# Kernel tuning notes

Hardware: AMD Instinct MI355X
Metric: run time of the kernel (lower is better)

The kernel has to match this reference:

```python
import jax, jax.numpy as jnp
import numpy as np

NUM_HEADS = 16
ROPE_BASE = 10000.0


def _rope_interleaved(x, cos, sin):
    # x: (B, S, H, hd); cos/sin: (1, S, 1, hd//2)
    x1 = x[..., ::2]
    x2 = x[..., 1::2]
    r1 = x1 * cos - x2 * sin
    r2 = x1 * sin + x2 * cos
    return jnp.stack([r1, r2], axis=-1).reshape(x.shape)


def _rope_tables(seq_len, head_dim, dtype):
    dim = head_dim // 2
    freqs = jnp.exp(-jnp.arange(0, dim, dtype=dtype) * jnp.log(jnp.asarray(ROPE_BASE, dtype)) / dim)
    pos = jnp.arange(seq_len, dtype=dtype)
    angles = pos[:, None] * freqs[None, :]  # (S, hd//2)
    return jnp.cos(angles)[None, :, None, :], jnp.sin(angles)[None, :, None, :]


def setup_inputs() -> dict:
    key = jax.random.key(0)
    ks = jax.random.split(key, 9)
    B, S, D = 2, 2048, 2048
    sc = 1.0 / np.sqrt(D)
    return {
        "x": jax.random.normal(ks[0], (B, S, D), jnp.float32),
        "wq": jax.random.normal(ks[1], (D, D), jnp.float32) * sc,
        "bq": jax.random.normal(ks[2], (D,), jnp.float32) * 0.01,
        "wk": jax.random.normal(ks[3], (D, D), jnp.float32) * sc,
        "bk": jax.random.normal(ks[4], (D,), jnp.float32) * 0.01,
        "wv": jax.random.normal(ks[5], (D, D), jnp.float32) * sc,
        "bv": jax.random.normal(ks[6], (D,), jnp.float32) * 0.01,
        "wo": jax.random.normal(ks[7], (D, D), jnp.float32) * sc,
        "bo": jax.random.normal(ks[8], (D,), jnp.float32) * 0.01,
    }


def reference(x, wq, bq, wk, bk, wv, bv, wo, bo):
    B, S, D = x.shape
    H = NUM_HEADS
    hd = D // H
    # QKV projections (eqx.nn.Linear: y = W @ x + b, weight (out, in))
    q = (x @ wq.T + bq).reshape(B, S, H, hd)
    k = (x @ wk.T + bk).reshape(B, S, H, hd)
    v = (x @ wv.T + bv).reshape(B, S, H, hd)
    # RoPE (interleaved / GPT-NeoX style)
    cos, sin = _rope_tables(S, hd, x.dtype)
    q = _rope_interleaved(q, cos, sin)
    k = _rope_interleaved(k, cos, sin)
    # Causal scaled dot-product attention
    scale = 1.0 / np.sqrt(hd)
    scores = jnp.einsum("bqhd,bkhd->bhqk", q, k) * scale
    causal = jnp.tril(jnp.ones((S, S), dtype=bool))
    scores = jnp.where(causal[None, None, :, :], scores, jnp.finfo(scores.dtype).min)
    attn = jax.nn.softmax(scores, axis=-1)
    out = jnp.einsum("bhqk,bkhd->bqhd", attn, v).reshape(B, S, D)
    return out @ wo.T + bo
```

## Files before the change

### kernel.cpp

```cpp
#include <hip/hip_runtime.h>

typedef unsigned short u16;
typedef short bf16x8 __attribute__((ext_vector_type(8)));
typedef float f32x4 __attribute__((ext_vector_type(4)));

#define B_ 2
#define S_ 2048
#define D_ 2048
#define HD_ 128
#define GW 512
#define KB 64
#define VST 72
#define PST 72

__device__ __forceinline__ float bf2f(u16 h) {
  unsigned u = ((unsigned)h) << 16;
  return __builtin_bit_cast(float, u);
}
__device__ __forceinline__ u16 f2bf(float f) {
  unsigned u = __builtin_bit_cast(unsigned, f);
  u += 0x7FFF + ((u >> 16) & 1);
  return (u16)(u >> 16);
}
__device__ __forceinline__ bf16x8 cvt8(const float* p) {
  float4 a = *(const float4*)p;
  float4 b = *(const float4*)(p + 4);
  bf16x8 r;
  r[0] = (short)f2bf(a.x); r[1] = (short)f2bf(a.y);
  r[2] = (short)f2bf(a.z); r[3] = (short)f2bf(a.w);
  r[4] = (short)f2bf(b.x); r[5] = (short)f2bf(b.y);
  r[6] = (short)f2bf(b.z); r[7] = (short)f2bf(b.w);
  return r;
}

__device__ __forceinline__ void gload16(const void* g, void* lds) {
  __builtin_amdgcn_global_load_lds(
      (const __attribute__((address_space(1))) unsigned*)g,
      (__attribute__((address_space(3))) unsigned*)lds, 16, 0, 0);
}

__device__ __forceinline__ f32x4 mfma16(bf16x8 a, bf16x8 b, f32x4 c) {
  return __builtin_amdgcn_mfma_f32_16x16x32_bf16(a, b, c, 0, 0, 0);
}

__global__ void k_cvt_all(const float* __restrict__ x, const float* __restrict__ wq,
                          const float* __restrict__ wk, const float* __restrict__ wv,
                          const float* __restrict__ wo, u16* __restrict__ xb,
                          u16* __restrict__ wqkvb, u16* wob, float2* tab) {
  const int slice = blockIdx.y;
  const int i = blockIdx.x * 256 + threadIdx.x;
  if (slice == 5) {
    if (tab != nullptr && i < 131072) {
      const int s = i >> 6, ip = i & 63;
      const float freq = expf(-(float)ip * 0.14391157f);
      float sv, cv;
      sincosf((float)s * freq, &sv, &cv);
      tab[i] = make_float2(cv, sv);
    }
    return;
  }
  if (slice == 4 && wob == nullptr) return;
  const float* src;
  u16* dst;
  int n8;
  if (slice == 0) { src = x; dst = xb; n8 = 1048576; }
  else if (slice == 1) { src = wq; dst = wqkvb; n8 = 524288; }
  else if (slice == 2) { src = wk; dst = wqkvb + 4194304; n8 = 524288; }
  else if (slice == 3) { src = wv; dst = wqkvb + 8388608; n8 = 524288; }
  else { src = wo; dst = wob; n8 = 524288; }
  if (i < n8) *(bf16x8*)(dst + (size_t)i * 8) = cvt8(src + (size_t)i * 8);
}

template <int AM, int WM, int CM>
__device__ __forceinline__ void gemm_body(const void* Ap, const void* Wp,
                                          const float* __restrict__ bias,
                                          void* Cp, int ldc,
                                          const float2* __restrict__ tab) {
  constexpr int K = 2048;
  __shared__ u16 As[128 * 32];
  __shared__ u16 Bs[128 * 32];
  const int t = threadIdx.x;
  const int w = t >> 6, l = t & 63, lr = l & 15, lg = l >> 4;
  const int m0 = blockIdx.y * 128, n0 = blockIdx.x * 128;
  const int wr = w >> 1, wc = w & 1;

  f32x4 acc[4][4];
#pragma unroll
  for (int i = 0; i < 4; ++i)
#pragma unroll
    for (int j = 0; j < 4; ++j) acc[i][j] = f32x4{0.f, 0.f, 0.f, 0.f};

  const int rowA0 = t >> 2, ko0 = (t & 3) * 8;
  const int rowA1 = (t + 256) >> 2, ko1 = ((t + 256) & 3) * 8;

  for (int kt = 0; kt < K; kt += 32) {
    if constexpr (AM == 1) {
      const u16* A = (const u16*)Ap;
      gload16(A + (size_t)(m0 + rowA0) * K + kt + ko0, (char*)As + (size_t)w * 1024);
      gload16(A + (size_t)(m0 + rowA1) * K + kt + ko1, (char*)As + (size_t)(w + 4) * 1024);
    } else {
      const float* A = (const float*)Ap;
      *(bf16x8*)((char*)As + (size_t)t * 16) = cvt8(A + (size_t)(m0 + rowA0) * K + kt + ko0);
      *(bf16x8*)((char*)As + (size_t)(t + 256) * 16) = cvt8(A + (size_t)(m0 + rowA1) * K + kt + ko1);
    }
    if constexpr (WM == 1) {
      const u16* W = (const u16*)Wp;
      gload16(W + (size_t)(n0 + rowA0) * K + kt + ko0, (char*)Bs + (size_t)w * 1024);
      gload16(W + (size_t)(n0 + rowA1) * K + kt + ko1, (char*)Bs + (size_t)(w + 4) * 1024);
    } else {
      const float* W = (const float*)Wp;
      *(bf16x8*)((char*)Bs + (size_t)t * 16) = cvt8(W + (size_t)(n0 + rowA0) * K + kt + ko0);
      *(bf16x8*)((char*)Bs + (size_t)(t + 256) * 16) = cvt8(W + (size_t)(n0 + rowA1) * K + kt + ko1);
    }
    __syncthreads();

    bf16x8 af[4], bw[4];
#pragma unroll
    for (int i = 0; i < 4; ++i) {
      af[i] = *(const bf16x8*)(As + (size_t)(wr * 64 + i * 16 + lr) * 32 + lg * 8);
      bw[i] = *(const bf16x8*)(Bs + (size_t)(wc * 64 + i * 16 + lr) * 32 + lg * 8);
    }
#pragma unroll
    for (int i = 0; i < 4; ++i)
#pragma unroll
      for (int j = 0; j < 4; ++j)
        acc[i][j] = mfma16(af[i], bw[j], acc[i][j]);
    __syncthreads();
  }

#pragma unroll
  for (int i = 0; i < 4; ++i) {
#pragma unroll
    for (int j = 0; j < 4; ++j) {
      const int col = n0 + wc * 64 + j * 16 + lr;
      const float bv = bias[col];
      const int row = m0 + wr * 64 + i * 16 + lg * 4;
      if (CM == 0 && tab != nullptr) {
        const int ip = (col & 127) >> 1;
        const int odd = col & 1;
#pragma unroll
        for (int r = 0; r < 4; ++r) {
          const float v = acc[i][j][r] + bv;
          const float p = __shfl_xor(v, 1, 64);
          const float2 cs = tab[((row + r) & (S_ - 1)) * 64 + ip];
          const float o = odd ? (p * cs.y + v * cs.x) : (v * cs.x - p * cs.y);
          ((u16*)Cp)[(size_t)(row + r) * ldc + col] = f2bf(o);
        }
      } else {
#pragma unroll
        for (int r = 0; r < 4; ++r) {
          if constexpr (CM == 1)
            ((float*)Cp)[(size_t)(row + r) * ldc + col] = acc[i][j][r] + bv;
          else
            ((u16*)Cp)[(size_t)(row + r) * ldc + col] = f2bf(acc[i][j][r] + bv);
        }
      }
    }
  }
}

__global__ __launch_bounds__(256) void k_gemm_qkv_bb(
    const u16* __restrict__ xb, const u16* __restrict__ wqkvb,
    const float* __restrict__ bq, const float* __restrict__ bk,
    const float* __restrict__ bv, u16* __restrict__ q, u16* __restrict__ k,
    u16* __restrict__ v, const float2* __restrict__ tab) {
  const int z = blockIdx.z;
  const u16* W = wqkvb + (size_t)z * D_ * D_;
  const float* bias = z == 0 ? bq : (z == 1 ? bk : bv);
  u16* C = z == 0 ? q : (z == 1 ? k : v);
  gemm_body<1, 1, 0>(xb, W, bias, C, D_, z == 2 ? nullptr : tab);
}

__global__ __launch_bounds__(256) void k_gemm_out_bb(
    const u16* __restrict__ ao, const u16* __restrict__ wob,
    const float* __restrict__ bo, float* __restrict__ out) {
  gemm_body<1, 1, 1>(ao, wob, bo, out, D_, nullptr);
}

__global__ __launch_bounds__(256) void k_gemm_qkv_xb(
    const u16* __restrict__ xb, const float* __restrict__ wq,
    const float* __restrict__ bq, const float* __restrict__ wk,
    const float* __restrict__ bk, const float* __restrict__ wv,
    const float* __restrict__ bv, u16* __restrict__ q, u16* __restrict__ k,
    u16* __restrict__ v) {
  const int z = blockIdx.z;
  const float* W = z == 0 ? wq : (z == 1 ? wk : wv);
  const float* bias = z == 0 ? bq : (z == 1 ? bk : bv);
  u16* C = z == 0 ? q : (z == 1 ? k : v);
  gemm_body<1, 0, 0>(xb, W, bias, C, D_, nullptr);
}

__global__ __launch_bounds__(256) void k_gemm_out(const u16* __restrict__ ao,
                                                  const float* __restrict__ wo,
                                                  const float* __restrict__ bo,
                                                  float* __restrict__ out) {
  gemm_body<1, 0, 1>(ao, wo, bo, out, D_, nullptr);
}

__global__ __launch_bounds__(256) void k_gemm_qkv_g(
    const float* __restrict__ x, const float* __restrict__ wq,
    const float* __restrict__ bq, const float* __restrict__ wk,
    const float* __restrict__ bk, const float* __restrict__ wv,
    const float* __restrict__ bv, u16* __restrict__ qg, u16* __restrict__ kg,
    u16* __restrict__ vg, int g) {
  const int z = blockIdx.z;
  const float* W = (z == 0 ? wq : (z == 1 ? wk : wv)) + (size_t)g * GW * D_;
  const float* bias = (z == 0 ? bq : (z == 1 ? bk : bv)) + g * GW;
  u16* C = z == 0 ? qg : (z == 1 ? kg : vg);
  gemm_body<0, 0, 0>(x, W, bias, C, GW, nullptr);
}

__device__ __forceinline__ void rope_one(u16* p, float cv, float sv) {
  unsigned u = *(const unsigned*)p;
  float x1 = bf2f((u16)(u & 0xffff)), x2 = bf2f((u16)(u >> 16));
  unsigned r = (unsigned)f2bf(x1 * cv - x2 * sv) |
               ((unsigned)f2bf(x1 * sv + x2 * cv) << 16);
  *(unsigned*)p = r;
}

__global__ void k_rope_full(u16* q, u16* kk) {
  const int idx = blockIdx.x * 256 + threadIdx.x;
  const int i = idx & 63;
  const int hh = (idx >> 6) & 15;
  const int bs = idx >> 10;
  const int s = bs & (S_ - 1);
  const float freq = expf(-(float)i * 0.14391157f);
  float sv, cv;
  sincosf((float)s * freq, &sv, &cv);
  const size_t off = (size_t)bs * D_ + (size_t)hh * HD_ + 2 * i;
  rope_one(q + off, cv, sv);
  rope_one(kk + off, cv, sv);
}

__global__ void k_rope_g(u16* q, u16* kk) {
  const int idx = blockIdx.x * 256 + threadIdx.x;
  const int i = idx & 63;
  const int hh = (idx >> 6) & 3;
  const int bs = idx >> 8;
  const int s = bs & (S_ - 1);
  const float freq = expf(-(float)i * 0.14391157f);
  float sv, cv;
  sincosf((float)s * freq, &sv, &cv);
  const size_t off = (size_t)bs * GW + (size_t)hh * HD_ + 2 * i;
  rope_one(q + off, cv, sv);
  rope_one(kk + off, cv, sv);
}

__device__ __forceinline__ void attn_body(const u16* Q, const u16* Kd,
                                          const u16* V, u16* O,
                                          size_t base_in, size_t base_out,
                                          int ld_in, int ld_out, int q0) {
  const int t = threadIdx.x, w = t >> 6, l = t & 63, lr = l & 15, lg = l >> 4;

  __shared__ u16 Ks[2][KB * HD_];
  __shared__ u16 Vt[2][HD_ * VST];
  __shared__ u16 Ps[4][16 * PST];

  bf16x8 qf[4];
  {
    const u16* qp = Q + base_in + (size_t)(q0 + w * 16 + lr) * ld_in;
#pragma unroll
    for (int ds = 0; ds < 4; ++ds)
      qf[ds] = *(const bf16x8*)(qp + ds * 32 + lg * 8);
  }

  f32x4 oacc[8];
#pragma unroll
  for (int f = 0; f < 8; ++f) oacc[f] = f32x4{0.f, 0.f, 0.f, 0.f};
  float mrow = -1e30f, lrow = 0.f;

  const int qrow = q0 + w * 16 + lr;
  const int nt = q0 / KB + 1;
  const float sc = 0.08838834764831845f;

  const int kRow = t >> 4, kC16 = t & 15;
  (void)kRow; (void)kC16;
  const int c1 = t + 256;
  const int kk20 = (t & 31) * 2, d00 = (t >> 5) * 8;
  const int kk21 = (c1 & 31) * 2, d01 = (c1 >> 5) * 8;

  bf16x8 vc[4];

#pragma unroll
  for (int r = 0; r < 4; ++r) {
    const int c = t + 256 * r;
    const int row = c >> 4, c16 = c & 15;
    const int gc = c16 ^ (row & 7);
    gload16(Kd + base_in + (size_t)row * ld_in + gc * 8,
            (char*)Ks[0] + (size_t)(w + 4 * r) * 1024);
  }
  vc[0] = *(const bf16x8*)(V + base_in + (size_t)kk20 * ld_in + d00);
  vc[1] = *(const bf16x8*)(V + base_in + (size_t)(kk20 + 1) * ld_in + d00);
  vc[2] = *(const bf16x8*)(V + base_in + (size_t)kk21 * ld_in + d01);
  vc[3] = *(const bf16x8*)(V + base_in + (size_t)(kk21 + 1) * ld_in + d01);

  for (int tt = 0; tt < nt; ++tt) {
    const int cur = tt & 1;
    const int kv0 = tt * KB;
    const bool more = (tt + 1 < nt);

    if (more) {
      const int kvn = kv0 + KB;
#pragma unroll
      for (int r = 0; r < 4; ++r) {
        const int c = t + 256 * r;
        const int row = c >> 4, c16 = c & 15;
        const int gc = c16 ^ (row & 7);
        gload16(Kd + base_in + (size_t)(kvn + row) * ld_in + gc * 8,
                (char*)Ks[cur ^ 1] + (size_t)(w + 4 * r) * 1024);
      }
      asm volatile("s_waitcnt vmcnt(4)" ::: "memory");
    } else {
      asm volatile("s_waitcnt vmcnt(0)" ::: "memory");
    }
    __builtin_amdgcn_sched_barrier(0);

    {
      u16* vt = Vt[cur];
#pragma unroll
      for (int j = 0; j < 8; ++j) {
        unsigned p0 = (unsigned)(unsigned short)vc[0][j] |
                      ((unsigned)(unsigned short)vc[1][j] << 16);
        *(unsigned*)&vt[(size_t)(d00 + j) * VST + kk20] = p0;
        unsigned p1 = (unsigned)(unsigned short)vc[2][j] |
                      ((unsigned)(unsigned short)vc[3][j] << 16);
        *(unsigned*)&vt[(size_t)(d01 + j) * VST + kk21] = p1;
      }
    }
    if (more) {
      const int kvn = kv0 + KB;
      vc[0] = *(const bf16x8*)(V + base_in + (size_t)(kvn + kk20) * ld_in + d00);
      vc[1] = *(const bf16x8*)(V + base_in + (size_t)(kvn + kk20 + 1) * ld_in + d00);
      vc[2] = *(const bf16x8*)(V + base_in + (size_t)(kvn + kk21) * ld_in + d01);
      vc[3] = *(const bf16x8*)(V + base_in + (size_t)(kvn + kk21 + 1) * ld_in + d01);
    }
    asm volatile("s_waitcnt lgkmcnt(0)" ::: "memory");
    __builtin_amdgcn_sched_barrier(0);
    __builtin_amdgcn_s_barrier();
    __builtin_amdgcn_sched_barrier(0);

    float p[16];
    __builtin_amdgcn_s_setprio(1);
#pragma unroll
    for (int h = 0; h < 4; ++h) {
      f32x4 s = {0.f, 0.f, 0.f, 0.f};
#pragma unroll
      for (int ds = 0; ds < 4; ++ds) {
        const int ch = (ds * 4 + lg) ^ (lr & 7);
        bf16x8 kf = *(const bf16x8*)(Ks[cur] + (size_t)(h * 16 + lr) * HD_ + ch * 8);
        s = mfma16(kf, qf[ds], s);
      }
#pragma unroll
      for (int r = 0; r < 4; ++r) p[h * 4 + r] = s[r] * sc;
    }
    __builtin_amdgcn_s_setprio(0);
    if (kv0 + KB - 1 > q0 + w * 16) {
#pragma unroll
      for (int h = 0; h < 4; ++h)
#pragma unroll
        for (int r = 0; r < 4; ++r)
          if (kv0 + h * 16 + lg * 4 + r > qrow) p[h * 4 + r] = -1e30f;
    }
    float pm = p[0];
#pragma unroll
    for (int i = 1; i < 16; ++i) pm = fmaxf(pm, p[i]);
    pm = fmaxf(pm, __shfl_xor(pm, 16, 64));
    pm = fmaxf(pm, __shfl_xor(pm, 32, 64));
    const float mn = fmaxf(mrow, pm);
    const float scl = __expf(mrow - mn);
    mrow = mn;
    float rs = 0.f;
#pragma unroll
    for (int i = 0; i < 16; ++i) {
      p[i] = __expf(p[i] - mn);
      rs += p[i];
    }
    rs += __shfl_xor(rs, 16, 64);
    rs += __shfl_xor(rs, 32, 64);
    lrow = lrow * scl + rs;
    float sj[4];
#pragma unroll
    for (int j = 0; j < 4; ++j) sj[j] = __shfl(scl, lg * 4 + j, 64);
#pragma unroll
    for (int f = 0; f < 8; ++f)
#pragma unroll
      for (int j = 0; j < 4; ++j) oacc[f][j] *= sj[j];
#pragma unroll
    for (int h = 0; h < 4; ++h)
#pragma unroll
      for (int r = 0; r < 4; ++r)
        Ps[w][lr * PST + h * 16 + lg * 4 + r] = f2bf(p[h * 4 + r]);
    bf16x8 pf0 = *(const bf16x8*)&Ps[w][lr * PST + lg * 8];
    bf16x8 pf1 = *(const bf16x8*)&Ps[w][lr * PST + 32 + lg * 8];
    __builtin_amdgcn_s_setprio(1);
#pragma unroll
    for (int f = 0; f < 8; ++f) {
      bf16x8 vf0 = *(const bf16x8*)&Vt[cur][(size_t)(f * 16 + lr) * VST + lg * 8];
      bf16x8 vf1 = *(const bf16x8*)&Vt[cur][(size_t)(f * 16 + lr) * VST + 32 + lg * 8];
      oacc[f] = mfma16(pf0, vf0, oacc[f]);
      oacc[f] = mfma16(pf1, vf1, oacc[f]);
    }
    __builtin_amdgcn_s_setprio(0);
    __builtin_amdgcn_sched_barrier(0);
    __builtin_amdgcn_s_barrier();
    __builtin_amdgcn_sched_barrier(0);
  }

  const float inv = 1.0f / lrow;
  float ij[4];
#pragma unroll
  for (int j = 0; j < 4; ++j) ij[j] = __shfl(inv, lg * 4 + j, 64);
  u16* Op = O + base_out;
#pragma unroll
  for (int f = 0; f < 8; ++f)
#pragma unroll
    for (int j = 0; j < 4; ++j)
      Op[(size_t)(q0 + w * 16 + lg * 4 + j) * ld_out + f * 16 + lr] =
          f2bf(oacc[f][j] * ij[j]);
}

__global__ __launch_bounds__(256) void k_attn_full(const u16* Q, const u16* Kd,
                                                   const u16* V, u16* O) {
  const int lin = blockIdx.y * gridDim.x + blockIdx.x;
  const int work = (lin & 7) * 64 + (lin >> 3);
  const int bh = work >> 4;
  const int pr = work & 15;
  const int b = bh >> 4, h = bh & 15;
  const size_t base = ((size_t)b * S_) * D_ + (size_t)h * HD_;
  attn_body(Q, Kd, V, O, base, base, D_, D_, 64 * (31 - pr));
  attn_body(Q, Kd, V, O, base, base, D_, D_, 64 * pr);
}

__global__ __launch_bounds__(256) void k_attn_g(const u16* __restrict__ Q,
                                                const u16* __restrict__ Kd,
                                                const u16* __restrict__ V,
                                                u16* __restrict__ O, int g) {
  const int by = blockIdx.y;
  const int b = by >> 2, hh = by & 3;
  const size_t base_in = ((size_t)b * S_) * GW + (size_t)hh * HD_;
  const size_t base_out = ((size_t)b * S_) * D_ + (size_t)(g * 4 + hh) * HD_;
  attn_body(Q, Kd, V, O, base_in, base_out, GW, D_, blockIdx.x * 64);
}

extern "C" void kernel_launch(void* const* d_in, const int* in_sizes, int n_in,
                              void* d_out, int out_size, void* d_ws,
                              size_t ws_size, hipStream_t stream) {
  (void)in_sizes; (void)n_in; (void)out_size;
  const float* x = (const float*)d_in[0];
  const float* wq = (const float*)d_in[1];
  const float* bq = (const float*)d_in[2];
  const float* wk = (const float*)d_in[3];
  const float* bk = (const float*)d_in[4];
  const float* wv = (const float*)d_in[5];
  const float* bv = (const float*)d_in[6];
  const float* wo = (const float*)d_in[7];
  const float* bo = (const float*)d_in[8];
  float* out = (float*)d_out;

  const size_t XB = (size_t)B_ * S_ * D_ * 2;
  const size_t WB3 = 3 * (size_t)D_ * D_ * 2;
  const size_t WB1 = (size_t)D_ * D_ * 2;
  const size_t TB = (size_t)S_ * 64 * 8;
  char* ws = (char*)d_ws;
  char* ob = (char*)d_out;

  u16 *xb, *q, *k, *v, *wqkvb = nullptr, *wob = nullptr;
  float2* tab = nullptr;
  int tier;
  if (ws_size >= 4 * XB + WB3 + WB1 + TB) {
    xb = (u16*)ws; q = (u16*)(ws + XB); k = (u16*)(ws + 2 * XB);
    v = (u16*)(ws + 3 * XB);
    wqkvb = (u16*)(ws + 4 * XB); wob = (u16*)(ws + 4 * XB + WB3);
    tab = (float2*)(ws + 4 * XB + WB3 + WB1);
    tier = 1;
  } else if (ws_size >= 3 * XB + WB3 + WB1 + TB) {
    xb = (u16*)ob;
    q = (u16*)ws; k = (u16*)(ws + XB); v = (u16*)(ws + 2 * XB);
    wqkvb = (u16*)(ws + 3 * XB); wob = (u16*)(ws + 3 * XB + WB3);
    tab = (float2*)(ws + 3 * XB + WB3 + WB1);
    tier = 1;
  } else if (ws_size >= 2 * XB + WB3 + TB) {
    xb = (u16*)ob; v = (u16*)(ob + XB);
    q = (u16*)ws; k = (u16*)(ws + XB);
    wqkvb = (u16*)(ws + 2 * XB);
    tab = (float2*)(ws + 2 * XB + WB3);
    tier = 2;
  } else if (ws_size >= 2 * XB) {
    xb = (u16*)ob; v = (u16*)(ob + XB);
    q = (u16*)ws; k = (u16*)(ws + XB);
    tier = 3;
  } else {
    tier = 4;
  }

  if (tier == 1 || tier == 2) {
    dim3 gc(4096, 6);
    k_cvt_all<<<gc, 256, 0, stream>>>(x, wq, wk, wv, wo, xb, wqkvb, wob, tab);
    dim3 g1(16, 32, 3);
    k_gemm_qkv_bb<<<g1, 256, 0, stream>>>(xb, wqkvb, bq, bk, bv, q, k, v, tab);
    dim3 g2(16, 32);
    k_attn_full<<<g2, 256, 0, stream>>>(q, k, v, q);
    dim3 g3(16, 32);
    if (tier == 1)
      k_gemm_out_bb<<<g3, 256, 0, stream>>>(q, wob, bo, out);
    else
      k_gemm_out<<<g3, 256, 0, stream>>>(q, wo, bo, out);
  } else if (tier == 3) {
    dim3 gc(4096, 1);
    k_cvt_all<<<gc, 256, 0, stream>>>(x, wq, wk, wv, wo, xb, xb, nullptr, nullptr);
    dim3 g1(16, 32, 3);
    k_gemm_qkv_xb<<<g1, 256, 0, stream>>>(xb, wq, bq, wk, bk, wv, bv, q, k, v);
    k_rope_full<<<16384, 256, 0, stream>>>(q, k);
    dim3 g2(16, 32);
    k_attn_full<<<g2, 256, 0, stream>>>(q, k, v, q);
    dim3 g3(16, 32);
    k_gemm_out<<<g3, 256, 0, stream>>>(q, wo, bo, out);
  } else {
    u16* qg = (u16*)ob;
    u16* kg = qg + (size_t)(B_ * S_) * GW;
    u16* vg = kg + (size_t)(B_ * S_) * GW;
    u16* ao = (u16*)ws;
    for (int g = 0; g < 4; ++g) {
      dim3 g1(4, 32, 3);
      k_gemm_qkv_g<<<g1, 256, 0, stream>>>(x, wq, bq, wk, bk, wv, bv, qg, kg, vg, g);
      k_rope_g<<<4096, 256, 0, stream>>>(qg, kg);
      dim3 g2(32, 8);
      k_attn_g<<<g2, 256, 0, stream>>>(qg, kg, vg, ao, g);
    }
    dim3 g3(16, 32);
    k_gemm_out<<<g3, 256, 0, stream>>>(ao, wo, bo, out);
  }
}
```

Measured before the change: 280.0 us.

## Add double-buffered 256x256 bf16 QKV GEMM kernel with direct-to-LDS loads

Replaces the 128x128, K=32 QKV projection GEMM with a new 512-thread kernel. It uses 256x256 output tiles, K=64 steps, double-buffered XOR-swizzled LDS filled by direct global-to-LDS loads, and raised wave priority around the MFMA blocks. RoPE stays fused in the epilogue. The larger tiles cut global traffic per FLOP and the double buffering overlaps loads with compute. The trade-off is about 128KB of LDS per block and only 384 blocks, which may leave CUs underused and create tail imbalance.

```diff
diff --git a/kernel.cpp b/kernel.cpp
--- a/kernel.cpp
+++ b/kernel.cpp
@@ -71,11 +71,116 @@
   if (i < n8) *(bf16x8*)(dst + (size_t)i * 8) = cvt8(src + (size_t)i * 8);
 }
 
+__global__ __launch_bounds__(512, 2) void k_gemm_qkv_256(
+    const u16* __restrict__ xb, const u16* __restrict__ wqkvb,
+    const float* __restrict__ bq, const float* __restrict__ bk,
+    const float* __restrict__ bv, u16* __restrict__ q, u16* __restrict__ k,
+    u16* __restrict__ v, const float2* __restrict__ tab) {
+  constexpr int K = 2048, NT = 32;
+  __shared__ u16 SA[2][256 * 64];
+  __shared__ u16 SB[2][256 * 64];
+  const int z = blockIdx.z;
+  const u16* W = wqkvb + (size_t)z * D_ * D_;
+  const float* bias = z == 0 ? bq : (z == 1 ? bk : bv);
+  u16* C = z == 0 ? q : (z == 1 ? k : v);
+  const float2* tb = z == 2 ? nullptr : tab;
+
+  const int t = threadIdx.x, wid = t >> 6, l = t & 63, lr = l & 15, lg = l >> 4;
+  const int wm = wid >> 2, wn = wid & 3;
+  const int m0 = blockIdx.y * 256, n0 = blockIdx.x * 256;
+
+  const int srow = wid * 8 + (l >> 3);
+  const int sc = (l & 7) ^ (srow & 7);
+
+  f32x4 acc[8][4];
+#pragma unroll
+  for (int i = 0; i < 8; ++i)
+#pragma unroll
+    for (int j = 0; j < 4; ++j) acc[i][j] = f32x4{0.f, 0.f, 0.f, 0.f};
+
+#pragma unroll
+  for (int r = 0; r < 4; ++r) {
+    const int row = r * 64 + srow;
+    gload16(xb + (size_t)(m0 + row) * K + sc * 8,
+            (void*)(SA[0] + (size_t)(r * 64 + wid * 8) * 64));
+    gload16(W + (size_t)(n0 + row) * K + sc * 8,
+            (void*)(SB[0] + (size_t)(r * 64 + wid * 8) * 64));
+  }
+  asm volatile("s_waitcnt vmcnt(0)" ::: "memory");
+  __builtin_amdgcn_sched_barrier(0);
+  __builtin_amdgcn_s_barrier();
+  __builtin_amdgcn_sched_barrier(0);
+
+  for (int tt = 0; tt < NT; ++tt) {
+    const int slot = tt & 1;
+    if (tt + 1 < NT) {
+      const int kt = (tt + 1) * 64;
+#pragma unroll
+      for (int r = 0; r < 4; ++r) {
+        const int row = r * 64 + srow;
+        gload16(xb + (size_t)(m0 + row) * K + kt + sc * 8,
+                (void*)(SA[slot ^ 1] + (size_t)(r * 64 + wid * 8) * 64));
+        gload16(W + (size_t)(n0 + row) * K + kt + sc * 8,
+                (void*)(SB[slot ^ 1] + (size_t)(r * 64 + wid * 8) * 64));
+      }
+    }
+    const u16* sa = SA[slot];
+    const u16* sb = SB[slot];
+#pragma unroll
+    for (int ks = 0; ks < 2; ++ks) {
+      const int ch = ((ks * 4 + lg) ^ (lr & 7)) * 8;
+      bf16x8 bf[4], af[8];
+#pragma unroll
+      for (int j = 0; j < 4; ++j)
+        bf[j] = *(const bf16x8*)(sb + (size_t)(wn * 64 + j * 16 + lr) * 64 + ch);
+#pragma unroll
+      for (int i = 0; i < 8; ++i)
+        af[i] = *(const bf16x8*)(sa + (size_t)(wm * 128 + i * 16 + lr) * 64 + ch);
+      __builtin_amdgcn_s_setprio(1);
+#pragma unroll
+      for (int i = 0; i < 8; ++i)
+#pragma unroll
+        for (int j = 0; j < 4; ++j)
+          acc[i][j] = mfma16(af[i], bf[j], acc[i][j]);
+      __builtin_amdgcn_s_setprio(0);
+    }
+    asm volatile("s_waitcnt vmcnt(0)" ::: "memory");
+    __builtin_amdgcn_sched_barrier(0);
+    __builtin_amdgcn_s_barrier();
+    __builtin_amdgcn_sched_barrier(0);
+  }
+
+#pragma unroll
+  for (int i = 0; i < 8; ++i) {
+#pragma unroll
+    for (int j = 0; j < 4; ++j) {
+      const int col = n0 + wn * 64 + j * 16 + lr;
+      const float bv_ = bias[col];
+      const int row = m0 + wm * 128 + i * 16 + lg * 4;
+      if (tb != nullptr) {
+        const int ip = (col & 127) >> 1;
+        const int odd = col & 1;
+#pragma unroll
+        for (int r = 0; r < 4; ++r) {
+          const float vv = acc[i][j][r] + bv_;
+          const float pp = __shfl_xor(vv, 1, 64);
+          const float2 cs = tb[((row + r) & (S_ - 1)) * 64 + ip];
+          const float o = odd ? (pp * cs.y + vv * cs.x) : (vv * cs.x - pp * cs.y);
+          C[(size_t)(row + r) * D_ + col] = f2bf(o);
+        }
+      } else {
+#pragma unroll
+        for (int r = 0; r < 4; ++r)
+          C[(size_t)(row + r) * D_ + col] = f2bf(acc[i][j][r] + bv_);
+      }
+    }
+  }
+}
+
 template <int AM, int WM, int CM>
 __device__ __forceinline__ void gemm_body(const void* Ap, const void* Wp,
                                           const float* __restrict__ bias,
-                                          void* Cp, int ldc,
-                                          const float2* __restrict__ tab) {
+                                          void* Cp, int ldc) {
   constexpr int K = 2048;
   __shared__ u16 As[128 * 32];
   __shared__ u16 Bs[128 * 32];
@@ -135,46 +240,21 @@
       const int col = n0 + wc * 64 + j * 16 + lr;
       const float bv = bias[col];
       const int row = m0 + wr * 64 + i * 16 + lg * 4;
-      if (CM == 0 && tab != nullptr) {
-        const int ip = (col & 127) >> 1;
-        const int odd = col & 1;
-#pragma unroll
-        for (int r = 0; r < 4; ++r) {
-          const float v = acc[i][j][r] + bv;
-          const float p = __shfl_xor(v, 1, 64);
-          const float2 cs = tab[((row + r) & (S_ - 1)) * 64 + ip];
-          const float o = odd ? (p * cs.y + v * cs.x) : (v * cs.x - p * cs.y);
-          ((u16*)Cp)[(size_t)(row + r) * ldc + col] = f2bf(o);
-        }
-      } else {
-#pragma unroll
-        for (int r = 0; r < 4; ++r) {
-          if constexpr (CM == 1)
-            ((float*)Cp)[(size_t)(row + r) * ldc + col] = acc[i][j][r] + bv;
-          else
-            ((u16*)Cp)[(size_t)(row + r) * ldc + col] = f2bf(acc[i][j][r] + bv);
-        }
+#pragma unroll
+      for (int r = 0; r < 4; ++r) {
+        if constexpr (CM == 1)
+          ((float*)Cp)[(size_t)(row + r) * ldc + col] = acc[i][j][r] + bv;
+        else
+          ((u16*)Cp)[(size_t)(row + r) * ldc + col] = f2bf(acc[i][j][r] + bv);
       }
     }
   }
-}
-
-__global__ __launch_bounds__(256) void k_gemm_qkv_bb(
-    const u16* __restrict__ xb, const u16* __restrict__ wqkvb,
-    const float* __restrict__ bq, const float* __restrict__ bk,
-    const float* __restrict__ bv, u16* __restrict__ q, u16* __restrict__ k,
-    u16* __restrict__ v, const float2* __restrict__ tab) {
-  const int z = blockIdx.z;
-  const u16* W = wqkvb + (size_t)z * D_ * D_;
-  const float* bias = z == 0 ? bq : (z == 1 ? bk : bv);
-  u16* C = z == 0 ? q : (z == 1 ? k : v);
-  gemm_body<1, 1, 0>(xb, W, bias, C, D_, z == 2 ? nullptr : tab);
 }
 
 __global__ __launch_bounds__(256) void k_gemm_out_bb(
     const u16* __restrict__ ao, const u16* __restrict__ wob,
     const float* __restrict__ bo, float* __restrict__ out) {
-  gemm_body<1, 1, 1>(ao, wob, bo, out, D_, nullptr);
+  gemm_body<1, 1, 1>(ao, wob, bo, out, D_);
 }
 
 __global__ __launch_bounds__(256) void k_gemm_qkv_xb(
@@ -187,14 +267,14 @@
   const float* W = z == 0 ? wq : (z == 1 ? wk : wv);
   const float* bias = z == 0 ? bq : (z == 1 ? bk : bv);
   u16* C = z == 0 ? q : (z == 1 ? k : v);
-  gemm_body<1, 0, 0>(xb, W, bias, C, D_, nullptr);
+  gemm_body<1, 0, 0>(xb, W, bias, C, D_);
 }
 
 __global__ __launch_bounds__(256) void k_gemm_out(const u16* __restrict__ ao,
                                                   const float* __restrict__ wo,
                                                   const float* __restrict__ bo,
                                                   float* __restrict__ out) {
-  gemm_body<1, 0, 1>(ao, wo, bo, out, D_, nullptr);
+  gemm_body<1, 0, 1>(ao, wo, bo, out, D_);
 }
 
 __global__ __launch_bounds__(256) void k_gemm_qkv_g(
@@ -207,7 +287,7 @@
   const float* W = (z == 0 ? wq : (z == 1 ? wk : wv)) + (size_t)g * GW * D_;
   const float* bias = (z == 0 ? bq : (z == 1 ? bk : bv)) + g * GW;
   u16* C = z == 0 ? qg : (z == 1 ? kg : vg);
-  gemm_body<0, 0, 0>(x, W, bias, C, GW, nullptr);
+  gemm_body<0, 0, 0>(x, W, bias, C, GW);
 }
 
 __device__ __forceinline__ void rope_one(u16* p, float cv, float sv) {
@@ -273,8 +353,6 @@
   const int nt = q0 / KB + 1;
   const float sc = 0.08838834764831845f;
 
-  const int kRow = t >> 4, kC16 = t & 15;
-  (void)kRow; (void)kC16;
   const int c1 = t + 256;
   const int kk20 = (t & 31) * 2, d00 = (t >> 5) * 8;
   const int kk21 = (c1 & 31) * 2, d01 = (c1 >> 5) * 8;
@@ -496,8 +574,8 @@
   if (tier == 1 || tier == 2) {
     dim3 gc(4096, 6);
     k_cvt_all<<<gc, 256, 0, stream>>>(x, wq, wk, wv, wo, xb, wqkvb, wob, tab);
-    dim3 g1(16, 32, 3);
-    k_gemm_qkv_bb<<<g1, 256, 0, stream>>>(xb, wqkvb, bq, bk, bv, q, k, v, tab);
+    dim3 g1(8, 16, 3);
+    k_gemm_qkv_256<<<g1, 512, 0, stream>>>(xb, wqkvb, bq, bk, bv, q, k, v, tab);
     dim3 g2(16, 32);
     k_attn_full<<<g2, 256, 0, stream>>>(q, k, v, q);
     dim3 g3(16, 32);
```

Measured after the change: 298.7 us. 6.7% more time.

## Share K/V tiles between paired query blocks in causal attention kernel

Applied to the files above, without the earlier changes.

The full attention kernel previously ran two independent attention passes per block, for a late and an early query tile, each loading its own K/V tiles. It now streams K/V once over the longer causal range and applies each loaded tile to both query tiles, stopping the second once its causal limit is reached. This halves K/V global loads and LDS staging for the early tile, at the cost of double the accumulator registers, which may reduce occupancy or cause spills.

```diff
diff --git a/kernel.cpp b/kernel.cpp
--- a/kernel.cpp
+++ b/kernel.cpp
@@ -273,8 +273,6 @@
   const int nt = q0 / KB + 1;
   const float sc = 0.08838834764831845f;
 
-  const int kRow = t >> 4, kC16 = t & 15;
-  (void)kRow; (void)kC16;
   const int c1 = t + 256;
   const int kk20 = (t & 31) * 2, d00 = (t >> 5) * 8;
   const int kk21 = (c1 & 31) * 2, d01 = (c1 >> 5) * 8;
@@ -419,6 +417,68 @@
           f2bf(oacc[f][j] * ij[j]);
 }
 
+#define TILE_COMPUTE(QT, QROW, QF, MROW, LROW, OACC)                           \
+  {                                                                            \
+    float p[16];                                                               \
+    __builtin_amdgcn_s_setprio(1);                                             \
+    _Pragma("unroll") for (int h = 0; h < 4; ++h) {                            \
+      f32x4 s = {0.f, 0.f, 0.f, 0.f};                                          \
+      _Pragma("unroll") for (int ds = 0; ds < 4; ++ds) {                       \
+        const int ch = (ds * 4 + lg) ^ (lr & 7);                               \
+        bf16x8 kf = *(const bf16x8*)(Ks[cur] +                                 \
+                                     (size_t)(h * 16 + lr) * HD_ + ch * 8);    \
+        s = mfma16(kf, QF[ds], s);                                             \
+      }                                                                        \
+      _Pragma("unroll") for (int r = 0; r < 4; ++r) p[h * 4 + r] = s[r] * sc;  \
+    }                                                                          \
+    __builtin_amdgcn_s_setprio(0);                                             \
+    if (kv0 + KB - 1 > (QT) + w * 16) {                                        \
+      _Pragma("unroll") for (int h = 0; h < 4; ++h)                            \
+          _Pragma("unroll") for (int r = 0; r < 4; ++r) if (kv0 + h * 16 +     \
+                                                            lg * 4 + r >      \
+                                                            (QROW))           \
+              p[h * 4 + r] = -1e30f;                                           \
+    }                                                                          \
+    float pm = p[0];                                                           \
+    _Pragma("unroll") for (int i = 1; i < 16; ++i) pm = fmaxf(pm, p[i]);       \
+    pm = fmaxf(pm, __shfl_xor(pm, 16, 64));                                    \
+    pm = fmaxf(pm, __shfl_xor(pm, 32, 64));                                    \
+    if (!__all(pm <= (MROW) + 8.f)) {                                          \
+      const float mn = fmaxf(MROW, pm);                                        \
+      const float scl = __expf((MROW)-mn);                                     \
+      MROW = mn;                                                               \
+      float sj[4];                                                             \
+      _Pragma("unroll") for (int j = 0; j < 4; ++j) sj[j] =                    \
+          __shfl(scl, lg * 4 + j, 64);                                         \
+      _Pragma("unroll") for (int f = 0; f < 8; ++f)                            \
+          _Pragma("unroll") for (int j = 0; j < 4; ++j) OACC[f][j] *= sj[j];   \
+      LROW *= scl;                                                             \
+    }                                                                          \
+    float rs = 0.f;                                                            \
+    _Pragma("unroll") for (int i = 0; i < 16; ++i) {                           \
+      p[i] = __expf(p[i] - (MROW));                                            \
+      rs += p[i];                                                              \
+    }                                                                          \
+    rs += __shfl_xor(rs, 16, 64);                                              \
+    rs += __shfl_xor(rs, 32, 64);                                              \
+    LROW += rs;                                                                \
+    _Pragma("unroll") for (int h = 0; h < 4; ++h)                              \
+        _Pragma("unroll") for (int r = 0; r < 4; ++r)                          \
+            Ps[w][lr * PST + h * 16 + lg * 4 + r] = f2bf(p[h * 4 + r]);        \
+    bf16x8 pf0 = *(const bf16x8*)&Ps[w][lr * PST + lg * 8];                    \
+    bf16x8 pf1 = *(const bf16x8*)&Ps[w][lr * PST + 32 + lg * 8];               \
+    __builtin_amdgcn_s_setprio(1);                                             \
+    _Pragma("unroll") for (int f = 0; f < 8; ++f) {                            \
+      bf16x8 vf0 =                                                             \
+          *(const bf16x8*)&Vt[cur][(size_t)(f * 16 + lr) * VST + lg * 8];      \
+      bf16x8 vf1 =                                                             \
+          *(const bf16x8*)&Vt[cur][(size_t)(f * 16 + lr) * VST + 32 + lg * 8]; \
+      OACC[f] = mfma16(pf0, vf0, OACC[f]);                                     \
+      OACC[f] = mfma16(pf1, vf1, OACC[f]);                                     \
+    }                                                                          \
+    __builtin_amdgcn_s_setprio(0);                                             \
+  }
+
 __global__ __launch_bounds__(256) void k_attn_full(const u16* Q, const u16* Kd,
                                                    const u16* V, u16* O) {
   const int lin = blockIdx.y * gridDim.x + blockIdx.x;
@@ -427,9 +487,139 @@
   const int pr = work & 15;
   const int b = bh >> 4, h = bh & 15;
   const size_t base = ((size_t)b * S_) * D_ + (size_t)h * HD_;
-  attn_body(Q, Kd, V, O, base, base, D_, D_, 64 * (31 - pr));
-  attn_body(Q, Kd, V, O, base, base, D_, D_, 64 * pr);
-}
+  const int qA = 64 * (31 - pr), qB = 64 * pr;
+
+  const int t = threadIdx.x, w = t >> 6, l = t & 63, lr = l & 15, lg = l >> 4;
+
+  __shared__ u16 Ks[2][KB * HD_];
+  __shared__ u16 Vt[2][HD_ * VST];
+  __shared__ u16 Ps[4][16 * PST];
+
+  bf16x8 qfA[4], qfB[4];
+  {
+    const u16* qp = Q + base + (size_t)(qA + w * 16 + lr) * D_;
+#pragma unroll
+    for (int ds = 0; ds < 4; ++ds)
+      qfA[ds] = *(const bf16x8*)(qp + ds * 32 + lg * 8);
+    qp = Q + base + (size_t)(qB + w * 16 + lr) * D_;
+#pragma unroll
+    for (int ds = 0; ds < 4; ++ds)
+      qfB[ds] = *(const bf16x8*)(qp + ds * 32 + lg * 8);
+  }
+
+  f32x4 oaccA[8], oaccB[8];
+#pragma unroll
+  for (int f = 0; f < 8; ++f) {
+    oaccA[f] = f32x4{0.f, 0.f, 0.f, 0.f};
+    oaccB[f] = f32x4{0.f, 0.f, 0.f, 0.f};
+  }
+  float mrowA = -1e30f, lrowA = 0.f, mrowB = -1e30f, lrowB = 0.f;
+  const int qrowA = qA + w * 16 + lr, qrowB = qB + w * 16 + lr;
+  const int ntA = qA / KB + 1;
+  const float sc = 0.08838834764831845f;
+
+  const int c1 = t + 256;
+  const int kk20 = (t & 31) * 2, d00 = (t >> 5) * 8;
+  const int kk21 = (c1 & 31) * 2, d01 = (c1 >> 5) * 8;
+
+  bf16x8 vc[4];
+
+#pragma unroll
+  for (int r = 0; r < 4; ++r) {
+    const int c = t + 256 * r;
+    const int row = c >> 4, c16 = c & 15;
+    const int gc = c16 ^ (row & 7);
+    gload16(Kd + base + (size_t)row * D_ + gc * 8,
+            (char*)Ks[0] + (size_t)(w + 4 * r) * 1024);
+  }
+  vc[0] = *(const bf16x8*)(V + base + (size_t)kk20 * D_ + d00);
+  vc[1] = *(const bf16x8*)(V + base + (size_t)(kk20 + 1) * D_ + d00);
+  vc[2] = *(const bf16x8*)(V + base + (size_t)kk21 * D_ + d01);
+  vc[3] = *(const bf16x8*)(V + base + (size_t)(kk21 + 1) * D_ + d01);
+
+  for (int tt = 0; tt < ntA; ++tt) {
+    const int cur = tt & 1;
+    const int kv0 = tt * KB;
+    const bool more = (tt + 1 < ntA);
+
+    if (more) {
+      const int kvn = kv0 + KB;
+#pragma unroll
+      for (int r = 0; r < 4; ++r) {
+        const int c = t + 256 * r;
+        const int row = c >> 4, c16 = c & 15;
+        const int gc = c16 ^ (row & 7);
+        gload16(Kd + base + (size_t)(kvn + row) * D_ + gc * 8,
+                (char*)Ks[cur ^ 1] + (size_t)(w + 4 * r) * 1024);
+      }
+      asm volatile("s_waitcnt vmcnt(4)" ::: "memory");
+    } else {
+      asm volatile("s_waitcnt vmcnt(0)" ::: "memory");
+    }
+    __builtin_amdgcn_sched_barrier(0);
+
+    {
+      u16* vt = Vt[cur];
+#pragma unroll
+      for (int j = 0; j < 8; ++j) {
+        unsigned p0 = (unsigned)(unsigned short)vc[0][j] |
+                      ((unsigned)(unsigned short)vc[1][j] << 16);
+        *(unsigned*)&vt[(size_t)(d00 + j) * VST + kk20] = p0;
+        unsigned p1 = (unsigned)(unsigned short)vc[2][j] |
+                      ((unsigned)(unsigned short)vc[3][j] << 16);
+        *(unsigned*)&vt[(size_t)(d01 + j) * VST + kk21] = p1;
+      }
+    }
+    if (more) {
+      const int kvn = kv0 + KB;
+      vc[0] = *(const bf16x8*)(V + base + (size_t)(kvn + kk20) * D_ + d00);
+      vc[1] = *(const bf16x8*)(V + base + (size_t)(kvn + kk20 + 1) * D_ + d00);
+      vc[2] = *(const bf16x8*)(V + base + (size_t)(kvn + kk21) * D_ + d01);
+      vc[3] = *(const bf16x8*)(V + base + (size_t)(kvn + kk21 + 1) * D_ + d01);
+    }
+    asm volatile("s_waitcnt lgkmcnt(0)" ::: "memory");
+    __builtin_amdgcn_sched_barrier(0);
+    __builtin_amdgcn_s_barrier();
+    __builtin_amdgcn_sched_barrier(0);
+
+    TILE_COMPUTE(qA, qrowA, qfA, mrowA, lrowA, oaccA);
+    if (tt <= pr) {
+      TILE_COMPUTE(qB, qrowB, qfB, mrowB, lrowB, oaccB);
+    }
+
+    __builtin_amdgcn_sched_barrier(0);
+    __builtin_amdgcn_s_barrier();
+    __builtin_amdgcn_sched_barrier(0);
+  }
+
+  {
+    const float inv = 1.0f / lrowA;
+    float ij[4];
+#pragma unroll
+    for (int j = 0; j < 4; ++j) ij[j] = __shfl(inv, lg * 4 + j, 64);
+    u16* Op = O + base;
+#pragma unroll
+    for (int f = 0; f < 8; ++f)
+#pragma unroll
+      for (int j = 0; j < 4; ++j)
+        Op[(size_t)(qA + w * 16 + lg * 4 + j) * D_ + f * 16 + lr] =
+            f2bf(oaccA[f][j] * ij[j]);
+  }
+  {
+    const float inv = 1.0f / lrowB;
+    float ij[4];
+#pragma unroll
+    for (int j = 0; j < 4; ++j) ij[j] = __shfl(inv, lg * 4 + j, 64);
+    u16* Op = O + base;
+#pragma unroll
+    for (int f = 0; f < 8; ++f)
+#pragma unroll
+      for (int j = 0; j < 4; ++j)
+        Op[(size_t)(qB + w * 16 + lg * 4 + j) * D_ + f * 16 + lr] =
+            f2bf(oaccB[f][j] * ij[j]);
+  }
+}
+#undef TILE_COMPUTE
 
 __global__ __launch_bounds__(256) void k_attn_g(const u16* __restrict__ Q,
                                                 const u16* __restrict__ Kd,
```

After: 276.6 us. Within noise of the previous version (-1.2%).
